# Performance work log

Measured on AMD Instinct MI355X. Metric: run time of the kernel, lower is better.

Reference implementation:

```python
import jax, jax.numpy as jnp
import numpy as np

TEMP = 0.7
EPS = 1e-6
LN_EPS = 1e-5
CAP_FACTOR = 2.0


def setup_inputs() -> dict:
    key = jax.random.key(0)
    B, S, H, E = 8, 4096, 2048, 8
    H2 = H // 2
    ks = jax.random.split(key, 3)
    x = jax.random.normal(ks[0], (B, S, H), jnp.float32)
    ln_w = jnp.ones((H,), jnp.float32)
    ln_b = jnp.zeros((H,), jnp.float32)
    # kaiming_normal_(fan_in, relu): std = sqrt(2 / fan_in)
    w1 = jax.random.normal(ks[1], (H2, H), jnp.float32) * np.float32(np.sqrt(2.0 / H))
    b1 = jnp.zeros((H2,), jnp.float32)
    w2 = jax.random.normal(ks[2], (E, H2), jnp.float32) * np.float32(np.sqrt(2.0 / H2))
    b2 = jnp.zeros((E,), jnp.float32)
    return {"x": x, "ln_w": ln_w, "ln_b": ln_b, "w1": w1, "b1": b1,
            "w2": w2, "b2": b2, "top_k": 2, "num_experts": E}


def _forward(x, ln_w, ln_b, w1, b1, w2, b2, top_k, num_experts):
    B, S, H = x.shape
    N = B * S
    # router: LayerNorm -> Linear -> GELU(exact) -> Linear
    mu = x.mean(-1, keepdims=True)
    var = jnp.mean((x - mu) ** 2, axis=-1, keepdims=True)
    h = (x - mu) * jax.lax.rsqrt(var + LN_EPS) * ln_w + ln_b
    h = jax.nn.gelu(h @ w1.T + b1, approximate=False)
    logits = h @ w2.T + b2
    ew = jnp.clip(logits / TEMP, -50.0, 50.0)  # [B,S,E]

    flat = ew.reshape(N, num_experts)
    capacity = int(CAP_FACTOR * N * top_k / num_experts)

    # top-k per token + softmax over the k selected logits, scatter into dense mask
    tk_w, tk_i = jax.lax.top_k(flat, top_k)          # [N,k]
    sm = jax.nn.softmax(tk_w, axis=-1)               # [N,k]
    rows = jnp.arange(N)[:, None]
    masks = jnp.zeros((N, num_experts), flat.dtype).at[rows, tk_i].set(sm)

    # capacity drop: per expert column, if sum of weights > capacity keep only
    # the top-`capacity` weighted tokens (extra zero-valued picks are no-ops,
    # matching the torch min(capacity, nnz) behavior).
    cols = masks.T                                   # [E,N]
    sums = cols.sum(-1)                              # [E]
    kcap = min(capacity, N)
    tv, ti = jax.lax.top_k(cols, kcap)               # [E,kcap]
    erow = jnp.arange(num_experts)[:, None]
    capped = jnp.zeros_like(cols).at[erow, ti].set(tv)
    over = sums > capacity
    cols = jnp.where(over[:, None], capped, cols)
    count = jax.lax.stop_gradient(jnp.where(over, capped.sum(-1), sums))  # buffer, no grad

    masks = cols.T
    masks = masks / jnp.maximum(masks.sum(-1, keepdims=True), EPS)

    usage = count / jnp.maximum(count.sum(), EPS)
    target = jnp.full((num_experts,), 1.0 / num_experts, usage.dtype)
    # F.kl_div(log(usage), target, reduction='batchmean') with batch dim = E
    kl = jnp.sum(target * (jnp.log(target) - jnp.log(jnp.maximum(usage, EPS)))) / num_experts
    loss = 0.01 * kl
    return ew, masks.reshape(B, S, num_experts), loss, usage


def reference(x, ln_w, ln_b, w1, b1, w2, b2, top_k, num_experts):
    return _forward(x, ln_w, ln_b, w1, b1, w2, b2, top_k, num_experts)
```

## Files before the change

### kernel.cpp

```cpp
#include <hip/hip_runtime.h>
#include <math.h>

#define NTOK 32768
#define HDIM 2048
#define H2DIM 1024
#define NE 8

#define WS_LOGITS 0
#define WS_SUMS 262144
#define WS_C1 262160
#define WS_C2 263184
#define WS_W1_BYTES 1057024ull
#define WS_NEED (WS_W1_BYTES + 8388608ull)

#define OUT_MASKS 262144
#define OUT_LOSS 524288
#define OUT_USAGE 524289

typedef _Float16 half8 __attribute__((ext_vector_type(8)));
typedef float floatx16 __attribute__((ext_vector_type(16)));

#define H_SCALE 0.03125f

#define GLDS16(g, l)                                                   \
  __builtin_amdgcn_global_load_lds(                                    \
      (const __attribute__((address_space(1))) void*)(g),              \
      (__attribute__((address_space(3))) void*)(l), 16, 0, 0)

__global__ __launch_bounds__(256) void w1prep_kernel(
    const float* __restrict__ w1, const float* __restrict__ ln_w,
    const float* __restrict__ ln_b, _Float16* __restrict__ w1p,
    float* __restrict__ ws) {
  const int tid = threadIdx.x;
  ((float4*)(ws + WS_LOGITS))[blockIdx.x * 256 + tid] =
      make_float4(0.f, 0.f, 0.f, 0.f);
  if (blockIdx.x == 0 && tid < NE) ws[WS_SUMS + tid] = 0.f;

  const int n = blockIdx.x * 4 + (tid >> 6);
  const int kc = tid & 63;
  const float4* src = (const float4*)(w1 + (size_t)n * HDIM + kc * 32);
  const float4* lwp = (const float4*)(ln_w + kc * 32);
  const float4* lbp = (const float4*)(ln_b + kc * 32);
  float wv[32], lwv[32], lbv[32];
#pragma unroll
  for (int v = 0; v < 8; ++v) {
    float4 f = src[v], g = lwp[v], h = lbp[v];
    wv[v*4+0]=f.x; wv[v*4+1]=f.y; wv[v*4+2]=f.z; wv[v*4+3]=f.w;
    lwv[v*4+0]=g.x; lwv[v*4+1]=g.y; lwv[v*4+2]=g.z; lwv[v*4+3]=g.w;
    lbv[v*4+0]=h.x; lbv[v*4+1]=h.y; lbv[v*4+2]=h.z; lbv[v*4+3]=h.w;
  }
  float c1 = 0.f, c2 = 0.f;
  _Float16 hi[32], lo[32];
#pragma unroll
  for (int v = 0; v < 32; ++v) {
    float wp = wv[v] * lwv[v];
    c1 += wp;
    c2 += lbv[v] * wv[v];
    float t = wp * 32.0f;
    hi[v] = (_Float16)t;
    lo[v] = (_Float16)((t - (float)hi[v]) * 4096.0f);
  }
  _Float16* dst = w1p + ((size_t)(n >> 5) * 64 + kc) * 2048;
  const int ln8 = (n & 31) * 8;
#pragma unroll
  for (int st = 0; st < 2; ++st)
#pragma unroll
    for (int f = 0; f < 2; ++f) {
      const int b = st * 16 + f * 8;
      half8 h = {hi[b+0],hi[b+1],hi[b+2],hi[b+3],hi[b+4],hi[b+5],hi[b+6],hi[b+7]};
      half8 l = {lo[b+0],lo[b+1],lo[b+2],lo[b+3],lo[b+4],lo[b+5],lo[b+6],lo[b+7]};
      *(half8*)&dst[st * 1024 + 0 + f * 256 + ln8] = h;
      *(half8*)&dst[st * 1024 + 512 + f * 256 + ln8] = l;
    }
#pragma unroll
  for (int o = 1; o < 64; o <<= 1) {
    c1 += __shfl_xor(c1, o);
    c2 += __shfl_xor(c2, o);
  }
  if (kc == 0) {
    ws[WS_C1 + n] = c1;
    ws[WS_C2 + n] = c2;
  }
}

__global__ __launch_bounds__(256, 3) void gemm_mfma_kernel(
    const float* __restrict__ x, const _Float16* __restrict__ w1p,
    const float* __restrict__ bias1, const float* __restrict__ w2,
    const float* __restrict__ C1, const float* __restrict__ C2,
    float* __restrict__ logits) {
  __shared__ _Float16 Abuf[8192];
  __shared__ _Float16 Bbuf[2][8192];
  __shared__ float sRow[128], sqRow[128];

  const int tid = threadIdx.x;
  const int lin = blockIdx.x;
  const int xcd = lin & 7, jj = lin >> 3;
  const int m0 = (xcd * 32 + (jj >> 3)) * 128;
  const int n0 = (jj & 7) * 128;

  const int lane = tid & 63;
  const int wid = tid >> 6;
  const int wm = wid >> 1, wn = wid & 1;
  const int fr = lane & 31, fq = lane >> 5;

  const int am = tid >> 1, st = tid & 1;
  const float* xrow = x + (size_t)(m0 + am) * HDIM + st * 16;
  _Float16* adst = Abuf + (am >> 5) * 2048 + st * 1024 + (am & 31) * 8;

  const _Float16* bsrc =
      w1p + ((size_t)((n0 >> 5) + wid) * 64) * 2048 + lane * 8;

  floatx16 acc[2][2];
#pragma unroll
  for (int i = 0; i < 2; ++i)
#pragma unroll
    for (int j = 0; j < 2; ++j)
#pragma unroll
      for (int r = 0; r < 16; ++r) acc[i][j][r] = 0.f;
  floatx16 zv;
#pragma unroll
  for (int r = 0; r < 16; ++r) zv[r] = 0.f;

  float s = 0.f, sq = 0.f;
  float4 xr0, xr1, xr2, xr3;
  {
    _Float16* bd = &Bbuf[0][wid * 2048];
    GLDS16(bsrc + 0, bd + 0);
    GLDS16(bsrc + 512, bd + 512);
    GLDS16(bsrc + 1024, bd + 1024);
    GLDS16(bsrc + 1536, bd + 1536);
    const float4* xp = (const float4*)xrow;
    xr0 = xp[0]; xr1 = xp[1]; xr2 = xp[2]; xr3 = xp[3];
  }

  for (int kc = 0; kc < 64; ++kc) {
    const int p = kc & 1;
    float xa[16] = {xr0.x,xr0.y,xr0.z,xr0.w, xr1.x,xr1.y,xr1.z,xr1.w,
                    xr2.x,xr2.y,xr2.z,xr2.w, xr3.x,xr3.y,xr3.z,xr3.w};
    _Float16 hi[16], lo[16];
#pragma unroll
    for (int v = 0; v < 16; ++v) {
      s += xa[v];
      sq = fmaf(xa[v], xa[v], sq);
      hi[v] = (_Float16)xa[v];
      lo[v] = (_Float16)((xa[v] - (float)hi[v]) * 4096.0f);
    }

    __syncthreads();
    {
      half8 h0 = {hi[0],hi[1],hi[2],hi[3],hi[4],hi[5],hi[6],hi[7]};
      half8 h1 = {hi[8],hi[9],hi[10],hi[11],hi[12],hi[13],hi[14],hi[15]};
      half8 l0 = {lo[0],lo[1],lo[2],lo[3],lo[4],lo[5],lo[6],lo[7]};
      half8 l1 = {lo[8],lo[9],lo[10],lo[11],lo[12],lo[13],lo[14],lo[15]};
      *(half8*)(adst + 0) = h0;
      *(half8*)(adst + 256) = h1;
      *(half8*)(adst + 512) = l0;
      *(half8*)(adst + 768) = l1;
    }
    __syncthreads();

    if (kc < 63) {
      const _Float16* bs = bsrc + (size_t)(kc + 1) * 2048;
      _Float16* bd = &Bbuf[p ^ 1][wid * 2048];
      GLDS16(bs + 0, bd + 0);
      GLDS16(bs + 512, bd + 512);
      GLDS16(bs + 1024, bd + 1024);
      GLDS16(bs + 1536, bd + 1536);
      const float4* xp = (const float4*)(xrow + (kc + 1) * 32);
      xr0 = xp[0]; xr1 = xp[1]; xr2 = xp[2]; xr3 = xp[3];
    }

#pragma unroll
    for (int t = 0; t < 2; ++t) {
      half8 ah[2], al[2], bh[2], bl[2];
#pragma unroll
      for (int i = 0; i < 2; ++i) {
        const int off = (wm * 2 + i) * 2048 + t * 1024 + lane * 8;
        ah[i] = *(const half8*)&Abuf[off];
        al[i] = *(const half8*)&Abuf[off + 512];
      }
#pragma unroll
      for (int j = 0; j < 2; ++j) {
        const int off = (wn * 2 + j) * 2048 + t * 1024 + lane * 8;
        bh[j] = *(const half8*)&Bbuf[p][off];
        bl[j] = *(const half8*)&Bbuf[p][off + 512];
      }
#pragma unroll
      for (int i = 0; i < 2; ++i)
#pragma unroll
        for (int j = 0; j < 2; ++j) {
          acc[i][j] = __builtin_amdgcn_mfma_f32_32x32x16_f16(ah[i], bh[j], acc[i][j], 0, 0, 0);
          floatx16 tmp = __builtin_amdgcn_mfma_f32_32x32x16_f16(ah[i], bl[j], zv, 0, 0, 0);
          tmp = __builtin_amdgcn_mfma_f32_32x32x16_f16(al[i], bh[j], tmp, 0, 0, 0);
          acc[i][j] += tmp * (1.0f / 4096.0f);
        }
    }
  }

  s += __shfl_xor(s, 1);
  sq += __shfl_xor(sq, 1);
  if (st == 0) { sRow[am] = s; sqRow[am] = sq; }
  __syncthreads();

  const float inv_sqrt2 = 0.70710678118654752440f;
  const int c = fr;
  const int col0 = n0 + wn * 64 + c;
  const int col1 = col0 + 32;
  float w2r0[NE], w2r1[NE];
#pragma unroll
  for (int e = 0; e < NE; ++e) {
    w2r0[e] = w2[e * H2DIM + col0];
    w2r1[e] = w2[e * H2DIM + col1];
  }
  const float c1a = C1[col0], c1b = C1[col1];
  const float hb0 = C2[col0] + bias1[col0];
  const float hb1 = C2[col1] + bias1[col1];

#pragma unroll
  for (int i = 0; i < 2; ++i)
#pragma unroll
    for (int r = 0; r < 16; ++r) {
      const int lr = wm * 64 + i * 32 + (r & 3) + 8 * (r >> 2) + 4 * fq;
      const float mu_r = sRow[lr] * (1.0f / HDIM);
      const float var =
          fmaxf(sqRow[lr] * (1.0f / HDIM) - mu_r * mu_r, 0.0f);
      const float rsr = 1.0f / sqrtf(var + 1e-5f);
      const float nmr = -rsr * mu_r;
      float h0 = fmaf(acc[i][0][r] * H_SCALE, rsr, fmaf(nmr, c1a, hb0));
      float h1 = fmaf(acc[i][1][r] * H_SCALE, rsr, fmaf(nmr, c1b, hb1));
      float g0 = 0.5f * h0 * (1.0f + erff(h0 * inv_sqrt2));
      float g1 = 0.5f * h1 * (1.0f + erff(h1 * inv_sqrt2));
      float pl[NE];
#pragma unroll
      for (int e = 0; e < NE; ++e) pl[e] = fmaf(g0, w2r0[e], g1 * w2r1[e]);
#pragma unroll
      for (int o = 1; o <= 16; o <<= 1)
#pragma unroll
        for (int e = 0; e < NE; ++e) pl[e] += __shfl_xor(pl[e], o);
      if (c == 0) {
        const int row = m0 + lr;
#pragma unroll
        for (int e = 0; e < NE; ++e)
          atomicAdd(&logits[(size_t)row * NE + e], pl[e]);
      }
    }
}

__global__ __launch_bounds__(256) void route_kernel(const float* __restrict__ logits,
                                                    const float* __restrict__ b2,
                                                    float* __restrict__ out,
                                                    float* __restrict__ sums) {
  __shared__ float ssum[NE];
  if (threadIdx.x < NE) ssum[threadIdx.x] = 0.f;
  __syncthreads();

  int tok = blockIdx.x * 256 + threadIdx.x;
  const float4* lp = (const float4*)(logits + (size_t)tok * NE);
  float4 l0 = lp[0], l1 = lp[1];
  float lv[NE] = {l0.x, l0.y, l0.z, l0.w, l1.x, l1.y, l1.z, l1.w};
  float ew[NE];
#pragma unroll
  for (int e = 0; e < NE; ++e) {
    float v = (lv[e] + b2[e]) / 0.7f;
    ew[e] = fminf(fmaxf(v, -50.0f), 50.0f);
  }

  int i1 = 0;
  float v1 = ew[0];
#pragma unroll
  for (int e = 1; e < NE; ++e)
    if (ew[e] > v1) { v1 = ew[e]; i1 = e; }
  int i2 = -1;
  float v2 = -1e30f;
#pragma unroll
  for (int e = 0; e < NE; ++e)
    if (e != i1 && ew[e] > v2) { v2 = ew[e]; i2 = e; }

  float t = expf(v2 - v1);
  float sm1 = 1.0f / (1.0f + t);
  float sm2 = t / (1.0f + t);
  float rsum = fmaxf(sm1 + sm2, 1e-6f);
  float m1 = sm1 / rsum, m2 = sm2 / rsum;

  float4* oew = (float4*)(out + (size_t)tok * NE);
  oew[0] = make_float4(ew[0], ew[1], ew[2], ew[3]);
  oew[1] = make_float4(ew[4], ew[5], ew[6], ew[7]);

  float mv[NE];
#pragma unroll
  for (int e = 0; e < NE; ++e)
    mv[e] = (e == i1) ? m1 : ((e == i2) ? m2 : 0.0f);
  float4* om = (float4*)(out + OUT_MASKS + (size_t)tok * NE);
  om[0] = make_float4(mv[0], mv[1], mv[2], mv[3]);
  om[1] = make_float4(mv[4], mv[5], mv[6], mv[7]);

  atomicAdd(&ssum[i1], sm1);
  atomicAdd(&ssum[i2], sm2);
  __syncthreads();
  if (threadIdx.x < NE) atomicAdd(&sums[threadIdx.x], ssum[threadIdx.x]);
}

__global__ void finalize_kernel(const float* __restrict__ sums,
                                float* __restrict__ out) {
  if (threadIdx.x != 0 || blockIdx.x != 0) return;
  float c[NE], tot = 0.f;
  for (int e = 0; e < NE; ++e) {
    c[e] = sums[e];
    tot += c[e];
  }
  float target = 1.0f / NE;
  float lt = logf(target);
  float kl = 0.f;
  for (int e = 0; e < NE; ++e) {
    float u = c[e] / fmaxf(tot, 1e-6f);
    out[OUT_USAGE + e] = u;
    kl += target * (lt - logf(fmaxf(u, 1e-6f)));
  }
  out[OUT_LOSS] = 0.01f * (kl / NE);
}

extern "C" void kernel_launch(void* const* d_in, const int* in_sizes, int n_in,
                              void* d_out, int out_size, void* d_ws, size_t ws_size,
                              hipStream_t stream) {
  const float* x = (const float*)d_in[0];
  const float* ln_w = (const float*)d_in[1];
  const float* ln_b = (const float*)d_in[2];
  const float* w1 = (const float*)d_in[3];
  const float* b1 = (const float*)d_in[4];
  const float* w2 = (const float*)d_in[5];
  const float* b2 = (const float*)d_in[6];
  float* out = (float*)d_out;
  float* ws = (float*)d_ws;
  _Float16* w1p = (_Float16*)((char*)d_ws + WS_W1_BYTES);
  (void)ws_size;

  w1prep_kernel<<<256, 256, 0, stream>>>(w1, ln_w, ln_b, w1p, ws);
  gemm_mfma_kernel<<<2048, 256, 0, stream>>>(
      x, w1p, b1, w2, ws + WS_C1, ws + WS_C2, ws + WS_LOGITS);
  route_kernel<<<NTOK / 256, 256, 0, stream>>>(ws + WS_LOGITS, b2, out,
                                               ws + WS_SUMS);
  finalize_kernel<<<1, 64, 0, stream>>>(ws + WS_SUMS, out);
}
```

Baseline: 1.145 ms.

## Double-buffer A tile, single barrier per step, separate low-part accumulator

After: 1.171 ms. +2.3%, slower.

```diff
diff --git a/kernel.cpp b/kernel.cpp
--- a/kernel.cpp
+++ b/kernel.cpp
@@ -83,12 +83,12 @@
   }
 }
 
-__global__ __launch_bounds__(256, 3) void gemm_mfma_kernel(
+__global__ __launch_bounds__(256, 2) void gemm_mfma_kernel(
     const float* __restrict__ x, const _Float16* __restrict__ w1p,
     const float* __restrict__ bias1, const float* __restrict__ w2,
     const float* __restrict__ C1, const float* __restrict__ C2,
     float* __restrict__ logits) {
-  __shared__ _Float16 Abuf[8192];
+  __shared__ _Float16 Abuf[2][8192];
   __shared__ _Float16 Bbuf[2][8192];
   __shared__ float sRow[128], sqRow[128];
 
@@ -105,60 +105,65 @@
 
   const int am = tid >> 1, st = tid & 1;
   const float* xrow = x + (size_t)(m0 + am) * HDIM + st * 16;
-  _Float16* adst = Abuf + (am >> 5) * 2048 + st * 1024 + (am & 31) * 8;
+  const int aoff = (am >> 5) * 2048 + st * 1024 + (am & 31) * 8;
 
   const _Float16* bsrc =
       w1p + ((size_t)((n0 >> 5) + wid) * 64) * 2048 + lane * 8;
 
-  floatx16 acc[2][2];
+  floatx16 acc[2][2], accL[2][2];
 #pragma unroll
   for (int i = 0; i < 2; ++i)
 #pragma unroll
     for (int j = 0; j < 2; ++j)
 #pragma unroll
-      for (int r = 0; r < 16; ++r) acc[i][j][r] = 0.f;
-  floatx16 zv;
-#pragma unroll
-  for (int r = 0; r < 16; ++r) zv[r] = 0.f;
+      for (int r = 0; r < 16; ++r) {
+        acc[i][j][r] = 0.f;
+        accL[i][j][r] = 0.f;
+      }
 
   float s = 0.f, sq = 0.f;
   float4 xr0, xr1, xr2, xr3;
+
+#define CVT_WRITE(dstbase)                                                    \
+  {                                                                           \
+    float xa[16] = {xr0.x, xr0.y, xr0.z, xr0.w, xr1.x, xr1.y, xr1.z, xr1.w,   \
+                    xr2.x, xr2.y, xr2.z, xr2.w, xr3.x, xr3.y, xr3.z, xr3.w};  \
+    _Float16 hi[16], lo[16];                                                  \
+    _Pragma("unroll") for (int v = 0; v < 16; ++v) {                          \
+      s += xa[v];                                                             \
+      sq = fmaf(xa[v], xa[v], sq);                                            \
+      hi[v] = (_Float16)xa[v];                                                \
+      lo[v] = (_Float16)((xa[v] - (float)hi[v]) * 4096.0f);                   \
+    }                                                                         \
+    half8 h0 = {hi[0], hi[1], hi[2],  hi[3],  hi[4],  hi[5],  hi[6],  hi[7]}; \
+    half8 h1 = {hi[8], hi[9], hi[10], hi[11], hi[12], hi[13], hi[14], hi[15]};\
+    half8 l0 = {lo[0], lo[1], lo[2],  lo[3],  lo[4],  lo[5],  lo[6],  lo[7]}; \
+    half8 l1 = {lo[8], lo[9], lo[10], lo[11], lo[12], lo[13], lo[14], lo[15]};\
+    *(half8*)((dstbase) + 0) = h0;                            \
+    *(half8*)((dstbase) + 256) = h1;                          \
+    *(half8*)((dstbase) + 512) = l0;                          \
+    *(half8*)((dstbase) + 768) = l1;                          \
+  }
+
   {
+    const float4* xp = (const float4*)xrow;
+    xr0 = xp[0]; xr1 = xp[1]; xr2 = xp[2]; xr3 = xp[3];
     _Float16* bd = &Bbuf[0][wid * 2048];
     GLDS16(bsrc + 0, bd + 0);
     GLDS16(bsrc + 512, bd + 512);
     GLDS16(bsrc + 1024, bd + 1024);
     GLDS16(bsrc + 1536, bd + 1536);
-    const float4* xp = (const float4*)xrow;
-    xr0 = xp[0]; xr1 = xp[1]; xr2 = xp[2]; xr3 = xp[3];
+    __builtin_amdgcn_sched_barrier(0);
+    CVT_WRITE(&Abuf[0][aoff]);
+    const float4* xq = (const float4*)(xrow + 32);
+    xr0 = xq[0]; xr1 = xq[1]; xr2 = xq[2]; xr3 = xq[3];
+    asm volatile("s_waitcnt vmcnt(4) lgkmcnt(0)" ::: "memory");
+    __builtin_amdgcn_s_barrier();
+    __builtin_amdgcn_sched_barrier(0);
   }
 
   for (int kc = 0; kc < 64; ++kc) {
     const int p = kc & 1;
-    float xa[16] = {xr0.x,xr0.y,xr0.z,xr0.w, xr1.x,xr1.y,xr1.z,xr1.w,
-                    xr2.x,xr2.y,xr2.z,xr2.w, xr3.x,xr3.y,xr3.z,xr3.w};
-    _Float16 hi[16], lo[16];
-#pragma unroll
-    for (int v = 0; v < 16; ++v) {
-      s += xa[v];
-      sq = fmaf(xa[v], xa[v], sq);
-      hi[v] = (_Float16)xa[v];
-      lo[v] = (_Float16)((xa[v] - (float)hi[v]) * 4096.0f);
-    }
-
-    __syncthreads();
-    {
-      half8 h0 = {hi[0],hi[1],hi[2],hi[3],hi[4],hi[5],hi[6],hi[7]};
-      half8 h1 = {hi[8],hi[9],hi[10],hi[11],hi[12],hi[13],hi[14],hi[15]};
-      half8 l0 = {lo[0],lo[1],lo[2],lo[3],lo[4],lo[5],lo[6],lo[7]};
-      half8 l1 = {lo[8],lo[9],lo[10],lo[11],lo[12],lo[13],lo[14],lo[15]};
-      *(half8*)(adst + 0) = h0;
-      *(half8*)(adst + 256) = h1;
-      *(half8*)(adst + 512) = l0;
-      *(half8*)(adst + 768) = l1;
-    }
-    __syncthreads();
-
     if (kc < 63) {
       const _Float16* bs = bsrc + (size_t)(kc + 1) * 2048;
       _Float16* bd = &Bbuf[p ^ 1][wid * 2048];
@@ -166,8 +171,12 @@
       GLDS16(bs + 512, bd + 512);
       GLDS16(bs + 1024, bd + 1024);
       GLDS16(bs + 1536, bd + 1536);
-      const float4* xp = (const float4*)(xrow + (kc + 1) * 32);
-      xr0 = xp[0]; xr1 = xp[1]; xr2 = xp[2]; xr3 = xp[3];
+      __builtin_amdgcn_sched_barrier(0);
+      CVT_WRITE(&Abuf[p ^ 1][aoff]);
+      if (kc < 62) {
+        const float4* xp = (const float4*)(xrow + (kc + 2) * 32);
+        xr0 = xp[0]; xr1 = xp[1]; xr2 = xp[2]; xr3 = xp[3];
+      }
     }
 
 #pragma unroll
@@ -176,8 +185,8 @@
 #pragma unroll
       for (int i = 0; i < 2; ++i) {
         const int off = (wm * 2 + i) * 2048 + t * 1024 + lane * 8;
-        ah[i] = *(const half8*)&Abuf[off];
-        al[i] = *(const half8*)&Abuf[off + 512];
+        ah[i] = *(const half8*)&Abuf[p][off];
+        al[i] = *(const half8*)&Abuf[p][off + 512];
       }
 #pragma unroll
       for (int j = 0; j < 2; ++j) {
@@ -185,15 +194,29 @@
         bh[j] = *(const half8*)&Bbuf[p][off];
         bl[j] = *(const half8*)&Bbuf[p][off + 512];
       }
+      __builtin_amdgcn_s_setprio(1);
 #pragma unroll
       for (int i = 0; i < 2; ++i)
 #pragma unroll
         for (int j = 0; j < 2; ++j) {
-          acc[i][j] = __builtin_amdgcn_mfma_f32_32x32x16_f16(ah[i], bh[j], acc[i][j], 0, 0, 0);
-          floatx16 tmp = __builtin_amdgcn_mfma_f32_32x32x16_f16(ah[i], bl[j], zv, 0, 0, 0);
-          tmp = __builtin_amdgcn_mfma_f32_32x32x16_f16(al[i], bh[j], tmp, 0, 0, 0);
-          acc[i][j] += tmp * (1.0f / 4096.0f);
+          acc[i][j] = __builtin_amdgcn_mfma_f32_32x32x16_f16(
+              ah[i], bh[j], acc[i][j], 0, 0, 0);
+          accL[i][j] = __builtin_amdgcn_mfma_f32_32x32x16_f16(
+              ah[i], bl[j], accL[i][j], 0, 0, 0);
+          accL[i][j] = __builtin_amdgcn_mfma_f32_32x32x16_f16(
+              al[i], bh[j], accL[i][j], 0, 0, 0);
         }
+      __builtin_amdgcn_s_setprio(0);
+    }
+
+    if (kc < 62) {
+      asm volatile("s_waitcnt vmcnt(4) lgkmcnt(0)" ::: "memory");
+      __builtin_amdgcn_s_barrier();
+      __builtin_amdgcn_sched_barrier(0);
+    } else if (kc == 62) {
+      asm volatile("s_waitcnt vmcnt(0) lgkmcnt(0)" ::: "memory");
+      __builtin_amdgcn_s_barrier();
+      __builtin_amdgcn_sched_barrier(0);
     }
   }
 
@@ -226,8 +249,10 @@
           fmaxf(sqRow[lr] * (1.0f / HDIM) - mu_r * mu_r, 0.0f);
       const float rsr = 1.0f / sqrtf(var + 1e-5f);
       const float nmr = -rsr * mu_r;
-      float h0 = fmaf(acc[i][0][r] * H_SCALE, rsr, fmaf(nmr, c1a, hb0));
-      float h1 = fmaf(acc[i][1][r] * H_SCALE, rsr, fmaf(nmr, c1b, hb1));
+      const float a0 = fmaf(accL[i][0][r], (1.0f / 4096.0f), acc[i][0][r]);
+      const float a1 = fmaf(accL[i][1][r], (1.0f / 4096.0f), acc[i][1][r]);
+      float h0 = fmaf(a0 * H_SCALE, rsr, fmaf(nmr, c1a, hb0));
+      float h1 = fmaf(a1 * H_SCALE, rsr, fmaf(nmr, c1b, hb1));
       float g0 = 0.5f * h0 * (1.0f + erff(h0 * inv_sqrt2));
       float g1 = 0.5f * h1 * (1.0f + erff(h1 * inv_sqrt2));
       float pl[NE];
```

## Load GEMM operands directly into registers, drop LDS staging and barriers

Applied to the files above, without the earlier changes.

New measurement: 1.148 ms. About the same (+0.3%).

```diff
diff --git a/kernel.cpp b/kernel.cpp
--- a/kernel.cpp
+++ b/kernel.cpp
@@ -21,11 +21,6 @@
 typedef float floatx16 __attribute__((ext_vector_type(16)));
 
 #define H_SCALE 0.03125f
-
-#define GLDS16(g, l)                                                   \
-  __builtin_amdgcn_global_load_lds(                                    \
-      (const __attribute__((address_space(1))) void*)(g),              \
-      (__attribute__((address_space(3))) void*)(l), 16, 0, 0)
 
 __global__ __launch_bounds__(256) void w1prep_kernel(
     const float* __restrict__ w1, const float* __restrict__ ln_w,
@@ -83,15 +78,52 @@
   }
 }
 
-__global__ __launch_bounds__(256, 3) void gemm_mfma_kernel(
+#define LDST(P, ks)                                                  \
+  P##a00 = *(const float4*)(pa0 + (size_t)(ks) * 16);                \
+  P##a01 = *(const float4*)(pa0 + (size_t)(ks) * 16 + 4);            \
+  P##a10 = *(const float4*)(pa1 + (size_t)(ks) * 16);                \
+  P##a11 = *(const float4*)(pa1 + (size_t)(ks) * 16 + 4);            \
+  P##bh0 = *(const half8*)(pb0 + (size_t)(ks) * 1024);               \
+  P##bl0 = *(const half8*)(pb0 + (size_t)(ks) * 1024 + 512);         \
+  P##bh1 = *(const half8*)(pb1 + (size_t)(ks) * 1024);               \
+  P##bl1 = *(const half8*)(pb1 + (size_t)(ks) * 1024 + 512);
+
+#define STEP(P)                                                               \
+  {                                                                           \
+    float f0[8] = {P##a00.x, P##a00.y, P##a00.z, P##a00.w,                    \
+                   P##a01.x, P##a01.y, P##a01.z, P##a01.w};                   \
+    float f1[8] = {P##a10.x, P##a10.y, P##a10.z, P##a10.w,                    \
+                   P##a11.x, P##a11.y, P##a11.z, P##a11.w};                   \
+    half8 ah0, al0, ah1, al1;                                                 \
+    _Pragma("unroll") for (int v = 0; v < 8; ++v) {                           \
+      sA[0] += f0[v]; sqA[0] = fmaf(f0[v], f0[v], sqA[0]);                    \
+      sA[1] += f1[v]; sqA[1] = fmaf(f1[v], f1[v], sqA[1]);                    \
+      ah0[v] = (_Float16)f0[v];                                               \
+      al0[v] = (_Float16)((f0[v] - (float)ah0[v]) * 4096.0f);                 \
+      ah1[v] = (_Float16)f1[v];                                               \
+      al1[v] = (_Float16)((f1[v] - (float)ah1[v]) * 4096.0f);                 \
+    }                                                                         \
+    __builtin_amdgcn_s_setprio(1);                                            \
+    acc[0][0] = __builtin_amdgcn_mfma_f32_32x32x16_f16(ah0, P##bh0, acc[0][0], 0, 0, 0);   \
+    accL[0][0] = __builtin_amdgcn_mfma_f32_32x32x16_f16(ah0, P##bl0, accL[0][0], 0, 0, 0); \
+    accL[0][0] = __builtin_amdgcn_mfma_f32_32x32x16_f16(al0, P##bh0, accL[0][0], 0, 0, 0); \
+    acc[0][1] = __builtin_amdgcn_mfma_f32_32x32x16_f16(ah0, P##bh1, acc[0][1], 0, 0, 0);   \
+    accL[0][1] = __builtin_amdgcn_mfma_f32_32x32x16_f16(ah0, P##bl1, accL[0][1], 0, 0, 0); \
+    accL[0][1] = __builtin_amdgcn_mfma_f32_32x32x16_f16(al0, P##bh1, accL[0][1], 0, 0, 0); \
+    acc[1][0] = __builtin_amdgcn_mfma_f32_32x32x16_f16(ah1, P##bh0, acc[1][0], 0, 0, 0);   \
+    accL[1][0] = __builtin_amdgcn_mfma_f32_32x32x16_f16(ah1, P##bl0, accL[1][0], 0, 0, 0); \
+    accL[1][0] = __builtin_amdgcn_mfma_f32_32x32x16_f16(al1, P##bh0, accL[1][0], 0, 0, 0); \
+    acc[1][1] = __builtin_amdgcn_mfma_f32_32x32x16_f16(ah1, P##bh1, acc[1][1], 0, 0, 0);   \
+    accL[1][1] = __builtin_amdgcn_mfma_f32_32x32x16_f16(ah1, P##bl1, accL[1][1], 0, 0, 0); \
+    accL[1][1] = __builtin_amdgcn_mfma_f32_32x32x16_f16(al1, P##bh1, accL[1][1], 0, 0, 0); \
+    __builtin_amdgcn_s_setprio(0);                                            \
+  }
+
+__global__ __launch_bounds__(256, 2) void gemm_mfma_kernel(
     const float* __restrict__ x, const _Float16* __restrict__ w1p,
     const float* __restrict__ bias1, const float* __restrict__ w2,
     const float* __restrict__ C1, const float* __restrict__ C2,
     float* __restrict__ logits) {
-  __shared__ _Float16 Abuf[8192];
-  __shared__ _Float16 Bbuf[2][8192];
-  __shared__ float sRow[128], sqRow[128];
-
   const int tid = threadIdx.x;
   const int lin = blockIdx.x;
   const int xcd = lin & 7, jj = lin >> 3;
@@ -103,104 +135,39 @@
   const int wm = wid >> 1, wn = wid & 1;
   const int fr = lane & 31, fq = lane >> 5;
 
-  const int am = tid >> 1, st = tid & 1;
-  const float* xrow = x + (size_t)(m0 + am) * HDIM + st * 16;
-  _Float16* adst = Abuf + (am >> 5) * 2048 + st * 1024 + (am & 31) * 8;
-
-  const _Float16* bsrc =
-      w1p + ((size_t)((n0 >> 5) + wid) * 64) * 2048 + lane * 8;
-
-  floatx16 acc[2][2];
+  const float* pa0 = x + (size_t)(m0 + wm * 64 + fr) * HDIM + fq * 8;
+  const float* pa1 = pa0 + (size_t)32 * HDIM;
+  const _Float16* pb0 =
+      w1p + ((size_t)((n0 >> 5) + wn * 2) * 64) * 2048 + lane * 8;
+  const _Float16* pb1 = pb0 + (size_t)64 * 2048;
+
+  floatx16 acc[2][2], accL[2][2];
 #pragma unroll
   for (int i = 0; i < 2; ++i)
 #pragma unroll
     for (int j = 0; j < 2; ++j)
 #pragma unroll
-      for (int r = 0; r < 16; ++r) acc[i][j][r] = 0.f;
-  floatx16 zv;
-#pragma unroll
-  for (int r = 0; r < 16; ++r) zv[r] = 0.f;
-
-  float s = 0.f, sq = 0.f;
-  float4 xr0, xr1, xr2, xr3;
-  {
-    _Float16* bd = &Bbuf[0][wid * 2048];
-    GLDS16(bsrc + 0, bd + 0);
-    GLDS16(bsrc + 512, bd + 512);
-    GLDS16(bsrc + 1024, bd + 1024);
-    GLDS16(bsrc + 1536, bd + 1536);
-    const float4* xp = (const float4*)xrow;
-    xr0 = xp[0]; xr1 = xp[1]; xr2 = xp[2]; xr3 = xp[3];
-  }
-
-  for (int kc = 0; kc < 64; ++kc) {
-    const int p = kc & 1;
-    float xa[16] = {xr0.x,xr0.y,xr0.z,xr0.w, xr1.x,xr1.y,xr1.z,xr1.w,
-                    xr2.x,xr2.y,xr2.z,xr2.w, xr3.x,xr3.y,xr3.z,xr3.w};
-    _Float16 hi[16], lo[16];
-#pragma unroll
-    for (int v = 0; v < 16; ++v) {
-      s += xa[v];
-      sq = fmaf(xa[v], xa[v], sq);
-      hi[v] = (_Float16)xa[v];
-      lo[v] = (_Float16)((xa[v] - (float)hi[v]) * 4096.0f);
-    }
-
-    __syncthreads();
-    {
-      half8 h0 = {hi[0],hi[1],hi[2],hi[3],hi[4],hi[5],hi[6],hi[7]};
-      half8 h1 = {hi[8],hi[9],hi[10],hi[11],hi[12],hi[13],hi[14],hi[15]};
-      half8 l0 = {lo[0],lo[1],lo[2],lo[3],lo[4],lo[5],lo[6],lo[7]};
-      half8 l1 = {lo[8],lo[9],lo[10],lo[11],lo[12],lo[13],lo[14],lo[15]};
-      *(half8*)(adst + 0) = h0;
-      *(half8*)(adst + 256) = h1;
-      *(half8*)(adst + 512) = l0;
-      *(half8*)(adst + 768) = l1;
-    }
-    __syncthreads();
-
-    if (kc < 63) {
-      const _Float16* bs = bsrc + (size_t)(kc + 1) * 2048;
-      _Float16* bd = &Bbuf[p ^ 1][wid * 2048];
-      GLDS16(bs + 0, bd + 0);
-      GLDS16(bs + 512, bd + 512);
-      GLDS16(bs + 1024, bd + 1024);
-      GLDS16(bs + 1536, bd + 1536);
-      const float4* xp = (const float4*)(xrow + (kc + 1) * 32);
-      xr0 = xp[0]; xr1 = xp[1]; xr2 = xp[2]; xr3 = xp[3];
-    }
-
-#pragma unroll
-    for (int t = 0; t < 2; ++t) {
-      half8 ah[2], al[2], bh[2], bl[2];
-#pragma unroll
-      for (int i = 0; i < 2; ++i) {
-        const int off = (wm * 2 + i) * 2048 + t * 1024 + lane * 8;
-        ah[i] = *(const half8*)&Abuf[off];
-        al[i] = *(const half8*)&Abuf[off + 512];
+      for (int r = 0; r < 16; ++r) {
+        acc[i][j][r] = 0.f;
+        accL[i][j][r] = 0.f;
       }
-#pragma unroll
-      for (int j = 0; j < 2; ++j) {
-        const int off = (wn * 2 + j) * 2048 + t * 1024 + lane * 8;
-        bh[j] = *(const half8*)&Bbuf[p][off];
-        bl[j] = *(const half8*)&Bbuf[p][off + 512];
-      }
-#pragma unroll
-      for (int i = 0; i < 2; ++i)
-#pragma unroll
-        for (int j = 0; j < 2; ++j) {
-          acc[i][j] = __builtin_amdgcn_mfma_f32_32x32x16_f16(ah[i], bh[j], acc[i][j], 0, 0, 0);
-          floatx16 tmp = __builtin_amdgcn_mfma_f32_32x32x16_f16(ah[i], bl[j], zv, 0, 0, 0);
-          tmp = __builtin_amdgcn_mfma_f32_32x32x16_f16(al[i], bh[j], tmp, 0, 0, 0);
-          acc[i][j] += tmp * (1.0f / 4096.0f);
-        }
-    }
-  }
-
-  s += __shfl_xor(s, 1);
-  sq += __shfl_xor(sq, 1);
-  if (st == 0) { sRow[am] = s; sqRow[am] = sq; }
-  __syncthreads();
+  float sA[2] = {0.f, 0.f}, sqA[2] = {0.f, 0.f};
+
+  float4 Ea00, Ea01, Ea10, Ea11, Oa00, Oa01, Oa10, Oa11;
+  half8 Ebh0, Ebl0, Ebh1, Ebl1, Obh0, Obl0, Obh1, Obl1;
+
+  LDST(E, 0);
+  for (int ks = 0; ks < 128; ks += 2) {
+    LDST(O, ks + 1);
+    STEP(E);
+    if (ks < 126) { LDST(E, ks + 2); }
+    STEP(O);
+  }
+
+  sA[0] += __shfl_xor(sA[0], 32);
+  sqA[0] += __shfl_xor(sqA[0], 32);
+  sA[1] += __shfl_xor(sA[1], 32);
+  sqA[1] += __shfl_xor(sqA[1], 32);
 
   const float inv_sqrt2 = 0.70710678118654752440f;
   const int c = fr;
@@ -220,14 +187,17 @@
   for (int i = 0; i < 2; ++i)
 #pragma unroll
     for (int r = 0; r < 16; ++r) {
-      const int lr = wm * 64 + i * 32 + (r & 3) + 8 * (r >> 2) + 4 * fq;
-      const float mu_r = sRow[lr] * (1.0f / HDIM);
-      const float var =
-          fmaxf(sqRow[lr] * (1.0f / HDIM) - mu_r * mu_r, 0.0f);
+      const int rr = (r & 3) + 8 * (r >> 2) + 4 * fq;
+      const float srow = __shfl(sA[i], rr);
+      const float sqrow = __shfl(sqA[i], rr);
+      const float mu_r = srow * (1.0f / HDIM);
+      const float var = fmaxf(sqrow * (1.0f / HDIM) - mu_r * mu_r, 0.0f);
       const float rsr = 1.0f / sqrtf(var + 1e-5f);
       const float nmr = -rsr * mu_r;
-      float h0 = fmaf(acc[i][0][r] * H_SCALE, rsr, fmaf(nmr, c1a, hb0));
-      float h1 = fmaf(acc[i][1][r] * H_SCALE, rsr, fmaf(nmr, c1b, hb1));
+      const float a0 = fmaf(accL[i][0][r], (1.0f / 4096.0f), acc[i][0][r]);
+      const float a1 = fmaf(accL[i][1][r], (1.0f / 4096.0f), acc[i][1][r]);
+      float h0 = fmaf(a0 * H_SCALE, rsr, fmaf(nmr, c1a, hb0));
+      float h1 = fmaf(a1 * H_SCALE, rsr, fmaf(nmr, c1b, hb1));
       float g0 = 0.5f * h0 * (1.0f + erff(h0 * inv_sqrt2));
       float g1 = 0.5f * h1 * (1.0f + erff(h1 * inv_sqrt2));
       float pl[NE];
@@ -238,7 +208,7 @@
 #pragma unroll
         for (int e = 0; e < NE; ++e) pl[e] += __shfl_xor(pl[e], o);
       if (c == 0) {
-        const int row = m0 + lr;
+        const int row = m0 + wm * 64 + i * 32 + rr;
 #pragma unroll
         for (int e = 0; e < NE; ++e)
           atomicAdd(&logits[(size_t)row * NE + e], pl[e]);
```
